# Performance work log

Measured on AMD Instinct MI355X. Metric: run time of the kernel, lower is better.

## Reference

```python
import jax, jax.numpy as jnp
import numpy as np

IN_F, OUT_F, RANK, ALPHA = 4096, 4096, 8, 32.0

def setup_inputs() -> dict:
    key = jax.random.key(0)
    kx, kw, ka, kb, kbias = jax.random.split(key, 5)
    x = jax.random.normal(kx, (4, 2048, IN_F), dtype=jnp.float32)
    weight = jax.random.normal(kw, (OUT_F, IN_F), dtype=jnp.float32) * 0.02
    a = jax.random.normal(ka, (OUT_F, RANK), dtype=jnp.float32) * 0.02
    b = jax.random.normal(kb, (RANK, IN_F), dtype=jnp.float32) * 0.02  # zeros in init; use randn for nontrivial test
    bias = jax.random.normal(kbias, (OUT_F,), dtype=jnp.float32) * 0.02
    return {"x": x, "weight": weight, "a": a, "b": b, "bias": bias}

def reference(x, weight, a, b, bias):
    # F.linear(x, W, bias) + F.linear(x, a @ b) * alpha / r
    base = jnp.einsum('bsi,oi->bso', x, weight) + bias
    # low-rank path computed in factored form (same math as x @ (a@b).T)
    lora = jnp.einsum('bsr,or->bso', jnp.einsum('bsi,ri->bsr', x, b), a)
    return base + lora * (ALPHA / RANK)
```

## Files before the change

### kernel.cpp

```cpp
#include <hip/hip_runtime.h>
#include <stdint.h>

#define IN_F 4096
#define OUT_F 4096
#define M_TOT 8192
#define LORA_SCALE 4.0f

typedef unsigned short u16;
typedef __attribute__((ext_vector_type(8))) short bf16x8;
typedef __attribute__((ext_vector_type(4))) float f32x4;

__device__ __forceinline__ u16 f2bf(float f) {
  union { float f; unsigned u; } v; v.f = f;
  unsigned r = v.u + 0x7FFFu + ((v.u >> 16) & 1u);
  return (u16)(r >> 16);
}

__device__ __forceinline__ void gload_lds16(const void* g, void* l) {
  __builtin_amdgcn_global_load_lds(
      (const __attribute__((address_space(1))) void*)g,
      (__attribute__((address_space(3))) void*)l, 16, 0, 0);
}

__global__ void merge_weight(const float* __restrict__ W,
                             const float* __restrict__ A,
                             const float* __restrict__ B,
                             u16* __restrict__ Wb) {
  int idx = blockIdx.x * blockDim.x + threadIdx.x;
  int o  = idx >> 10;
  int i0 = (idx & 1023) << 2;
  const float4 w = *(const float4*)(W + (size_t)o * IN_F + i0);
  float a0 = w.x, a1 = w.y, a2 = w.z, a3 = w.w;
#pragma unroll
  for (int r = 0; r < 8; ++r) {
    float ar = A[o * 8 + r] * LORA_SCALE;
    const float4 bv = *(const float4*)(B + (size_t)r * IN_F + i0);
    a0 += ar * bv.x; a1 += ar * bv.y; a2 += ar * bv.z; a3 += ar * bv.w;
  }
  uint2 pk;
  pk.x = (unsigned)f2bf(a0) | ((unsigned)f2bf(a1) << 16);
  pk.y = (unsigned)f2bf(a2) | ((unsigned)f2bf(a3) << 16);
  *(uint2*)(Wb + (size_t)o * IN_F + i0) = pk;
}

__global__ void convert_x(const float* __restrict__ X, u16* __restrict__ Xb) {
  size_t base = ((size_t)blockIdx.x * blockDim.x + threadIdx.x) * 8;
  float4 v0 = *(const float4*)(X + base);
  float4 v1 = *(const float4*)(X + base + 4);
  uint4 pk;
  pk.x = (unsigned)f2bf(v0.x) | ((unsigned)f2bf(v0.y) << 16);
  pk.y = (unsigned)f2bf(v0.z) | ((unsigned)f2bf(v0.w) << 16);
  pk.z = (unsigned)f2bf(v1.x) | ((unsigned)f2bf(v1.y) << 16);
  pk.w = (unsigned)f2bf(v1.z) | ((unsigned)f2bf(v1.w) << 16);
  *(uint4*)(Xb + base) = pk;
}


#define ABASE(b) ((b) * 32768)
#define BBASE(b) ((b) * 32768 + 16384)

#define STAGE_A(b, h, kt) do { \
  gload_lds16(aG + (size_t)((h) * 128) * IN_F + (kt),      lds + ABASE(b) + ((h) * 128) * 64      + tid * 8); \
  gload_lds16(aG + (size_t)((h) * 128 + 64) * IN_F + (kt), lds + ABASE(b) + ((h) * 128 + 64) * 64 + tid * 8); \
} while (0)

#define STAGE_B(b, h, kt) do { \
  gload_lds16(bG + (size_t)((h) * 128) * IN_F + (kt),      lds + BBASE(b) + ((h) * 128) * 64      + tid * 8); \
  gload_lds16(bG + (size_t)((h) * 128 + 64) * IN_F + (kt), lds + BBASE(b) + ((h) * 128 + 64) * 64 + tid * 8); \
} while (0)

#define WAIT4 asm volatile("s_waitcnt vmcnt(4)")
#define WAIT0 asm volatile("s_waitcnt vmcnt(0)")

#define PHASE(b, p, STAGE_STMT, WAIT_STMT) do { \
  if ((p) == 0) { \
    _Pragma("unroll") \
    for (int n = 0; n < 4; ++n) { \
      Bf0[n] = *(const bf16x8*)(lds + BBASE(b) + (rB + n * 16) * 64 + ck0); \
      Bf1[n] = *(const bf16x8*)(lds + BBASE(b) + (rB + n * 16) * 64 + ck1); \
    } \
  } \
  bf16x8 a00 = *(const bf16x8*)(lds + ABASE(b) + (rA + (2 * (p)) * 16) * 64 + ck0); \
  bf16x8 a01 = *(const bf16x8*)(lds + ABASE(b) + (rA + (2 * (p)) * 16) * 64 + ck1); \
  bf16x8 a10 = *(const bf16x8*)(lds + ABASE(b) + (rA + (2 * (p) + 1) * 16) * 64 + ck0); \
  bf16x8 a11 = *(const bf16x8*)(lds + ABASE(b) + (rA + (2 * (p) + 1) * 16) * 64 + ck1); \
  STAGE_STMT; \
  __builtin_amdgcn_s_barrier(); \
  asm volatile("s_waitcnt lgkmcnt(0)"); \
  __builtin_amdgcn_s_setprio(1); \
  _Pragma("unroll") \
  for (int n = 0; n < 4; ++n) { \
    acc[2 * (p)][n]     = __builtin_amdgcn_mfma_f32_16x16x32_bf16(a00, Bf0[n], acc[2 * (p)][n], 0, 0, 0); \
    acc[2 * (p) + 1][n] = __builtin_amdgcn_mfma_f32_16x16x32_bf16(a10, Bf0[n], acc[2 * (p) + 1][n], 0, 0, 0); \
  } \
  _Pragma("unroll") \
  for (int n = 0; n < 4; ++n) { \
    acc[2 * (p)][n]     = __builtin_amdgcn_mfma_f32_16x16x32_bf16(a01, Bf1[n], acc[2 * (p)][n], 0, 0, 0); \
    acc[2 * (p) + 1][n] = __builtin_amdgcn_mfma_f32_16x16x32_bf16(a11, Bf1[n], acc[2 * (p) + 1][n], 0, 0, 0); \
  } \
  __builtin_amdgcn_s_setprio(0); \
  WAIT_STMT; \
  __builtin_amdgcn_s_barrier(); \
} while (0)

__global__ __launch_bounds__(512, 2) void gemm8(const u16* __restrict__ Xb,
                                                const u16* __restrict__ Wb,
                                                const float* __restrict__ bias,
                                                float* __restrict__ out) {
  extern __shared__ u16 lds[];

  const int tid  = threadIdx.x;
  const int lane = tid & 63;
  const int wid  = tid >> 6;
  const int wr = wid >> 2, wc = wid & 3;
  const int lr = lane & 15, kg = lane >> 4;

  const int bid = blockIdx.x;
  const int swz = (bid & 7) * 64 + (bid >> 3);
  const int mt = swz >> 4, nt = swz & 15;
  const int m0 = mt * 256, n0 = nt * 256;

  const int srow = tid >> 3;
  const int swc  = (tid & 7) ^ (srow & 7);
  const u16* aG = Xb + (size_t)(m0 + srow) * IN_F + swc * 8;
  const u16* bG = Wb + (size_t)(n0 + srow) * IN_F + swc * 8;

  const int rA = wr * 128 + lr;
  const int rB = wc * 64 + lr;
  const int ck0 = ((kg) ^ (lane & 7)) * 8;
  const int ck1 = ((4 + kg) ^ (lane & 7)) * 8;

  f32x4 acc[8][4] = {};
  bf16x8 Bf0[4], Bf1[4];

  STAGE_B(0, 0, 0); STAGE_B(0, 1, 0);
  STAGE_A(0, 0, 0); STAGE_A(0, 1, 0);
  STAGE_B(1, 0, 64); STAGE_B(1, 1, 64);
  WAIT4;
  __builtin_amdgcn_s_barrier();

  for (int i = 0; i < 31; ++i) {
    const int kt1 = i * 128 + 64, kt2 = i * 128 + 128, kt3 = i * 128 + 192;
    PHASE(0, 0, STAGE_A(1, 0, kt1), );
    PHASE(0, 1, STAGE_A(1, 1, kt1), );
    PHASE(0, 2, STAGE_B(0, 0, kt2), );
    PHASE(0, 3, STAGE_B(0, 1, kt2), WAIT4);
    PHASE(1, 0, STAGE_A(0, 0, kt2), );
    PHASE(1, 1, STAGE_A(0, 1, kt2), );
    PHASE(1, 2, STAGE_B(1, 0, kt3), );
    PHASE(1, 3, STAGE_B(1, 1, kt3), WAIT4);
  }
  PHASE(0, 0, STAGE_A(1, 0, 4032), );
  PHASE(0, 1, STAGE_A(1, 1, 4032), );
  PHASE(0, 2, , );
  PHASE(0, 3, , WAIT0);
  PHASE(1, 0, , );
  PHASE(1, 1, , );
  PHASE(1, 2, , );
  PHASE(1, 3, , );

  float bv[4];
#pragma unroll
  for (int n = 0; n < 4; ++n) bv[n] = bias[n0 + wc * 64 + n * 16 + lr];
  const int rbase = m0 + wr * 128 + kg * 4;
#pragma unroll
  for (int m = 0; m < 8; ++m)
#pragma unroll
    for (int n = 0; n < 4; ++n) {
      int col = n0 + wc * 64 + n * 16 + lr;
#pragma unroll
      for (int r = 0; r < 4; ++r)
        out[(size_t)(rbase + m * 16 + r) * OUT_F + col] = acc[m][n][r] + bv[n];
    }
}

__global__ __launch_bounds__(256) void gemm_bias(const u16* __restrict__ Xb,
                                                 const u16* __restrict__ Wb,
                                                 const float* __restrict__ bias,
                                                 float* __restrict__ out) {
  __shared__ __align__(16) u16 ldsA[128 * 64];
  __shared__ __align__(16) u16 ldsB[128 * 64];

  const int tid  = threadIdx.x;
  const int wid  = tid >> 6;
  const int lane = tid & 63;
  const int nt = blockIdx.x & 31;
  const int mt = blockIdx.x >> 5;
  const int m0 = mt * 128, n0 = nt * 128;
  const int wr = wid >> 1, wc = wid & 1;
  const int lr = lane & 15;
  const int kg = lane >> 4;

  const int srow   = wid * 8 + (lane >> 3);
  const int schunk = (lane & 7) ^ (srow & 7);
  const u16* aSrc = Xb + (size_t)(m0 + srow) * IN_F + schunk * 8;
  const u16* bSrc = Wb + (size_t)(n0 + srow) * IN_F + schunk * 8;

  f32x4 acc[4][4] = {};

  for (int kt = 0; kt < IN_F; kt += 64) {
    __syncthreads();
#pragma unroll
    for (int j = 0; j < 4; ++j) {
      gload_lds16(aSrc + (size_t)(j * 32) * IN_F + kt, &ldsA[j * 2048 + wid * 512]);
      gload_lds16(bSrc + (size_t)(j * 32) * IN_F + kt, &ldsB[j * 2048 + wid * 512]);
    }
    __syncthreads();

#pragma unroll
    for (int s = 0; s < 2; ++s) {
      bf16x8 af[4], bfr[4];
#pragma unroll
      for (int m = 0; m < 4; ++m) {
        int r = wr * 64 + m * 16 + lr;
        int c = (s * 4 + kg) ^ (r & 7);
        af[m] = *(const bf16x8*)&ldsA[r * 64 + c * 8];
      }
#pragma unroll
      for (int n = 0; n < 4; ++n) {
        int r = wc * 64 + n * 16 + lr;
        int c = (s * 4 + kg) ^ (r & 7);
        bfr[n] = *(const bf16x8*)&ldsB[r * 64 + c * 8];
      }
#pragma unroll
      for (int m = 0; m < 4; ++m)
#pragma unroll
        for (int n = 0; n < 4; ++n)
          acc[m][n] = __builtin_amdgcn_mfma_f32_16x16x32_bf16(af[m], bfr[n], acc[m][n], 0, 0, 0);
    }
  }

  float bv[4];
#pragma unroll
  for (int n = 0; n < 4; ++n) bv[n] = bias[n0 + wc * 64 + n * 16 + lr];
  const int rbase = m0 + wr * 64 + kg * 4;
#pragma unroll
  for (int m = 0; m < 4; ++m)
#pragma unroll
    for (int n = 0; n < 4; ++n) {
      int col = n0 + wc * 64 + n * 16 + lr;
#pragma unroll
      for (int r = 0; r < 4; ++r)
        out[(size_t)(rbase + m * 16 + r) * OUT_F + col] = acc[m][n][r] + bv[n];
    }
}

__global__ void lora_t(const float* __restrict__ x, const float* __restrict__ B,
                       float* __restrict__ t) {
  int m = blockIdx.x;
  int tid = threadIdx.x, lane = tid & 63;
  float p[8] = {0, 0, 0, 0, 0, 0, 0, 0};
  for (int k = tid; k < IN_F; k += 256) {
    float xv = x[(size_t)m * IN_F + k];
#pragma unroll
    for (int r = 0; r < 8; ++r) p[r] += xv * B[r * IN_F + k];
  }
#pragma unroll
  for (int r = 0; r < 8; ++r) {
    float v = p[r];
    for (int off = 32; off; off >>= 1) v += __shfl_down(v, off);
    if (lane == 0) atomicAdd(&t[m * 8 + r], v);
  }
}

__global__ void fb_gemm(const float* __restrict__ x, const float* __restrict__ W,
                        const float* __restrict__ A, const float* __restrict__ bias,
                        const float* __restrict__ t, float* __restrict__ out) {
  __shared__ float sx[64][17];
  __shared__ float sw[64][17];
  int tx = threadIdx.x, ty = threadIdx.y;
  int tid = ty * 16 + tx;
  int m0 = blockIdx.y * 64, n0 = blockIdx.x * 64;
  float acc[4][4] = {};
  for (int kt = 0; kt < IN_F; kt += 16) {
    __syncthreads();
#pragma unroll
    for (int q = 0; q < 4; ++q) {
      int idx = q * 256 + tid;
      int r = idx >> 4, c = idx & 15;
      sx[r][c] = x[(size_t)(m0 + r) * IN_F + kt + c];
      sw[r][c] = W[(size_t)(n0 + r) * IN_F + kt + c];
    }
    __syncthreads();
#pragma unroll
    for (int k = 0; k < 16; ++k) {
      float xv[4], wv[4];
#pragma unroll
      for (int i = 0; i < 4; ++i) xv[i] = sx[ty * 4 + i][k];
#pragma unroll
      for (int j = 0; j < 4; ++j) wv[j] = sw[tx * 4 + j][k];
#pragma unroll
      for (int i = 0; i < 4; ++i)
#pragma unroll
        for (int j = 0; j < 4; ++j) acc[i][j] += xv[i] * wv[j];
    }
  }
#pragma unroll
  for (int i = 0; i < 4; ++i) {
    int m = m0 + ty * 4 + i;
    float tv[8];
#pragma unroll
    for (int r = 0; r < 8; ++r) tv[r] = t[m * 8 + r];
#pragma unroll
    for (int j = 0; j < 4; ++j) {
      int o = n0 + tx * 4 + j;
      float lora = 0.f;
#pragma unroll
      for (int r = 0; r < 8; ++r) lora += tv[r] * A[o * 8 + r];
      out[(size_t)m * OUT_F + o] = acc[i][j] + bias[o] + LORA_SCALE * lora;
    }
  }
}

extern "C" void kernel_launch(void* const* d_in, const int* in_sizes, int n_in,
                              void* d_out, int out_size, void* d_ws, size_t ws_size,
                              hipStream_t stream) {
  const float* x    = (const float*)d_in[0];
  const float* W    = (const float*)d_in[1];
  const float* A    = (const float*)d_in[2];
  const float* B    = (const float*)d_in[3];
  const float* bias = (const float*)d_in[4];
  float* out = (float*)d_out;

  const size_t xb_elems = (size_t)M_TOT * IN_F;
  const size_t wb_elems = (size_t)OUT_F * IN_F;
  const size_t need = (xb_elems + wb_elems) * sizeof(u16);

  if (ws_size >= need) {
    u16* Xb = (u16*)d_ws;
    u16* Wb = Xb + xb_elems;
    merge_weight<<<(OUT_F * IN_F / 4) / 256, 256, 0, stream>>>(W, A, B, Wb);
    convert_x<<<(M_TOT * IN_F / 8) / 256, 256, 0, stream>>>(x, Xb);

    hipError_t e = hipFuncSetAttribute((const void*)gemm8,
                                       hipFuncAttributeMaxDynamicSharedMemorySize,
                                       131072);
    bool used8 = false;
    if (e == hipSuccess) {
      gemm8<<<512, 512, 131072, stream>>>(Xb, Wb, bias, out);
      used8 = (hipGetLastError() == hipSuccess);
    }
    if (!used8) {
      gemm_bias<<<(M_TOT / 128) * (OUT_F / 128), 256, 0, stream>>>(Xb, Wb, bias, out);
    }
  } else {
    float* t = (float*)d_ws;
    hipMemsetAsync(t, 0, (size_t)M_TOT * 8 * sizeof(float), stream);
    lora_t<<<M_TOT, 256, 0, stream>>>(x, B, t);
    fb_gemm<<<dim3(OUT_F / 64, M_TOT / 64), dim3(16, 16), 0, stream>>>(x, W, A, bias, t, out);
  }
}
```

Measured before the change: 299.7 us.

## Halve GEMM phase barriers, fuse prep kernels, add nontemporal loads and stores

The GEMM main loop now uses a single barrier at the start of each phase instead of two per phase. It drops the explicit lgkmcnt wait and hoists the vmcnt waits out of the phase macro, with a sched_barrier to stop the compiler reordering across it. The weight merge and x-to-bf16 conversion kernels are fused into one launch with a split grid, and the streaming loads of x and W plus the output stores use nontemporal hints. The aim is less barrier stall time in the MFMA loop, one fewer launch, and less cache pollution. The risk is that the looser synchronisation leaves an LDS race if any reads or writes escape the single barrier.

```diff
diff --git a/kernel.cpp b/kernel.cpp
--- a/kernel.cpp
+++ b/kernel.cpp
@@ -22,37 +22,38 @@
       (__attribute__((address_space(3))) void*)l, 16, 0, 0);
 }
 
-__global__ void merge_weight(const float* __restrict__ W,
-                             const float* __restrict__ A,
-                             const float* __restrict__ B,
-                             u16* __restrict__ Wb) {
-  int idx = blockIdx.x * blockDim.x + threadIdx.x;
-  int o  = idx >> 10;
-  int i0 = (idx & 1023) << 2;
-  const float4 w = *(const float4*)(W + (size_t)o * IN_F + i0);
-  float a0 = w.x, a1 = w.y, a2 = w.z, a3 = w.w;
-#pragma unroll
-  for (int r = 0; r < 8; ++r) {
-    float ar = A[o * 8 + r] * LORA_SCALE;
-    const float4 bv = *(const float4*)(B + (size_t)r * IN_F + i0);
-    a0 += ar * bv.x; a1 += ar * bv.y; a2 += ar * bv.z; a3 += ar * bv.w;
-  }
-  uint2 pk;
-  pk.x = (unsigned)f2bf(a0) | ((unsigned)f2bf(a1) << 16);
-  pk.y = (unsigned)f2bf(a2) | ((unsigned)f2bf(a3) << 16);
-  *(uint2*)(Wb + (size_t)o * IN_F + i0) = pk;
-}
-
-__global__ void convert_x(const float* __restrict__ X, u16* __restrict__ Xb) {
-  size_t base = ((size_t)blockIdx.x * blockDim.x + threadIdx.x) * 8;
-  float4 v0 = *(const float4*)(X + base);
-  float4 v1 = *(const float4*)(X + base + 4);
-  uint4 pk;
-  pk.x = (unsigned)f2bf(v0.x) | ((unsigned)f2bf(v0.y) << 16);
-  pk.y = (unsigned)f2bf(v0.z) | ((unsigned)f2bf(v0.w) << 16);
-  pk.z = (unsigned)f2bf(v1.x) | ((unsigned)f2bf(v1.y) << 16);
-  pk.w = (unsigned)f2bf(v1.z) | ((unsigned)f2bf(v1.w) << 16);
-  *(uint4*)(Xb + base) = pk;
+__global__ void prep(const float* __restrict__ X, const float* __restrict__ W,
+                     const float* __restrict__ A, const float* __restrict__ B,
+                     u16* __restrict__ Xb, u16* __restrict__ Wb) {
+  int bid = blockIdx.x;
+  if (bid < 16384) {
+    size_t base = ((size_t)bid * blockDim.x + threadIdx.x) * 8;
+    const f32x4* p = (const f32x4*)(X + base);
+    f32x4 v0 = __builtin_nontemporal_load(p);
+    f32x4 v1 = __builtin_nontemporal_load(p + 1);
+    uint4 pk;
+    pk.x = (unsigned)f2bf(v0.x) | ((unsigned)f2bf(v0.y) << 16);
+    pk.y = (unsigned)f2bf(v0.z) | ((unsigned)f2bf(v0.w) << 16);
+    pk.z = (unsigned)f2bf(v1.x) | ((unsigned)f2bf(v1.y) << 16);
+    pk.w = (unsigned)f2bf(v1.z) | ((unsigned)f2bf(v1.w) << 16);
+    *(uint4*)(Xb + base) = pk;
+  } else {
+    int idx = (bid - 16384) * blockDim.x + threadIdx.x;
+    int o  = idx >> 10;
+    int i0 = (idx & 1023) << 2;
+    const f32x4 w = __builtin_nontemporal_load((const f32x4*)(W + (size_t)o * IN_F + i0));
+    float a0 = w.x, a1 = w.y, a2 = w.z, a3 = w.w;
+#pragma unroll
+    for (int r = 0; r < 8; ++r) {
+      float ar = A[o * 8 + r] * LORA_SCALE;
+      const float4 bv = *(const float4*)(B + (size_t)r * IN_F + i0);
+      a0 += ar * bv.x; a1 += ar * bv.y; a2 += ar * bv.z; a3 += ar * bv.w;
+    }
+    uint2 pk;
+    pk.x = (unsigned)f2bf(a0) | ((unsigned)f2bf(a1) << 16);
+    pk.y = (unsigned)f2bf(a2) | ((unsigned)f2bf(a3) << 16);
+    *(uint2*)(Wb + (size_t)o * IN_F + i0) = pk;
+  }
 }
 
 
@@ -69,10 +70,12 @@
   gload_lds16(bG + (size_t)((h) * 128 + 64) * IN_F + (kt), lds + BBASE(b) + ((h) * 128 + 64) * 64 + tid * 8); \
 } while (0)
 
-#define WAIT4 asm volatile("s_waitcnt vmcnt(4)")
-#define WAIT0 asm volatile("s_waitcnt vmcnt(0)")
-
-#define PHASE(b, p, STAGE_STMT, WAIT_STMT) do { \
+#define WAIT4 asm volatile("s_waitcnt vmcnt(4)" ::: "memory")
+#define WAIT0 asm volatile("s_waitcnt vmcnt(0)" ::: "memory")
+
+#define PHASE(b, p, STAGE_STMT) do { \
+  __builtin_amdgcn_s_barrier(); \
+  __builtin_amdgcn_sched_barrier(0); \
   if ((p) == 0) { \
     _Pragma("unroll") \
     for (int n = 0; n < 4; ++n) { \
@@ -85,8 +88,6 @@
   bf16x8 a10 = *(const bf16x8*)(lds + ABASE(b) + (rA + (2 * (p) + 1) * 16) * 64 + ck0); \
   bf16x8 a11 = *(const bf16x8*)(lds + ABASE(b) + (rA + (2 * (p) + 1) * 16) * 64 + ck1); \
   STAGE_STMT; \
-  __builtin_amdgcn_s_barrier(); \
-  asm volatile("s_waitcnt lgkmcnt(0)"); \
   __builtin_amdgcn_s_setprio(1); \
   _Pragma("unroll") \
   for (int n = 0; n < 4; ++n) { \
@@ -99,8 +100,6 @@
     acc[2 * (p) + 1][n] = __builtin_amdgcn_mfma_f32_16x16x32_bf16(a11, Bf1[n], acc[2 * (p) + 1][n], 0, 0, 0); \
   } \
   __builtin_amdgcn_s_setprio(0); \
-  WAIT_STMT; \
-  __builtin_amdgcn_s_barrier(); \
 } while (0)
 
 __global__ __launch_bounds__(512, 2) void gemm8(const u16* __restrict__ Xb,
@@ -137,27 +136,29 @@
   STAGE_A(0, 0, 0); STAGE_A(0, 1, 0);
   STAGE_B(1, 0, 64); STAGE_B(1, 1, 64);
   WAIT4;
-  __builtin_amdgcn_s_barrier();
 
   for (int i = 0; i < 31; ++i) {
     const int kt1 = i * 128 + 64, kt2 = i * 128 + 128, kt3 = i * 128 + 192;
-    PHASE(0, 0, STAGE_A(1, 0, kt1), );
-    PHASE(0, 1, STAGE_A(1, 1, kt1), );
-    PHASE(0, 2, STAGE_B(0, 0, kt2), );
-    PHASE(0, 3, STAGE_B(0, 1, kt2), WAIT4);
-    PHASE(1, 0, STAGE_A(0, 0, kt2), );
-    PHASE(1, 1, STAGE_A(0, 1, kt2), );
-    PHASE(1, 2, STAGE_B(1, 0, kt3), );
-    PHASE(1, 3, STAGE_B(1, 1, kt3), WAIT4);
-  }
-  PHASE(0, 0, STAGE_A(1, 0, 4032), );
-  PHASE(0, 1, STAGE_A(1, 1, 4032), );
-  PHASE(0, 2, , );
-  PHASE(0, 3, , WAIT0);
-  PHASE(1, 0, , );
-  PHASE(1, 1, , );
-  PHASE(1, 2, , );
-  PHASE(1, 3, , );
+    PHASE(0, 0, STAGE_A(1, 0, kt1));
+    PHASE(0, 1, STAGE_A(1, 1, kt1));
+    PHASE(0, 2, STAGE_B(0, 0, kt2));
+    PHASE(0, 3, STAGE_B(0, 1, kt2));
+    WAIT4;
+    PHASE(1, 0, STAGE_A(0, 0, kt2));
+    PHASE(1, 1, STAGE_A(0, 1, kt2));
+    PHASE(1, 2, STAGE_B(1, 0, kt3));
+    PHASE(1, 3, STAGE_B(1, 1, kt3));
+    WAIT4;
+  }
+  PHASE(0, 0, STAGE_A(1, 0, 4032));
+  PHASE(0, 1, STAGE_A(1, 1, 4032));
+  PHASE(0, 2, );
+  PHASE(0, 3, );
+  WAIT0;
+  PHASE(1, 0, );
+  PHASE(1, 1, );
+  PHASE(1, 2, );
+  PHASE(1, 3, );
 
   float bv[4];
 #pragma unroll
@@ -170,7 +171,8 @@
       int col = n0 + wc * 64 + n * 16 + lr;
 #pragma unroll
       for (int r = 0; r < 4; ++r)
-        out[(size_t)(rbase + m * 16 + r) * OUT_F + col] = acc[m][n][r] + bv[n];
+        __builtin_nontemporal_store(acc[m][n][r] + bv[n],
+                                    &out[(size_t)(rbase + m * 16 + r) * OUT_F + col]);
     }
 }
 
@@ -329,8 +331,7 @@
   if (ws_size >= need) {
     u16* Xb = (u16*)d_ws;
     u16* Wb = Xb + xb_elems;
-    merge_weight<<<(OUT_F * IN_F / 4) / 256, 256, 0, stream>>>(W, A, B, Wb);
-    convert_x<<<(M_TOT * IN_F / 8) / 256, 256, 0, stream>>>(x, Xb);
+    prep<<<32768, 256, 0, stream>>>(x, W, A, B, Xb, Wb);
 
     hipError_t e = hipFuncSetAttribute((const void*)gemm8,
                                        hipFuncAttributeMaxDynamicSharedMemorySize,
@@ -345,7 +346,7 @@
     }
   } else {
     float* t = (float*)d_ws;
-    hipMemsetAsync(t, 0, (size_t)M_TOT * 8 * sizeof(float), stream);
+    (void)hipMemsetAsync(t, 0, (size_t)M_TOT * 8 * sizeof(float), stream);
     lora_t<<<M_TOT, 256, 0, stream>>>(x, B, t);
     fb_gemm<<<dim3(OUT_F / 64, M_TOT / 64), dim3(16, 16), 0, stream>>>(x, W, A, bias, t, out);
   }
```

Result: no change. 294.7 us (-1.7%).
